# Optimization experiments

Measured on AMD Instinct MI355X. Metric: run time of the kernel, lower is better.

The kernel has to match this reference:

```python
import jax, jax.numpy as jnp
import numpy as np

N_NODES = 50000
N_EDGES = 1600000
IN_CH = 512
OUT_CH = 64
ITERATIONS = 3


def _spmm(adj_index, adj_values, x):
    # sparse @ dense: out[r] = sum_{e: row[e]==r} vals[e] * x[col[e]]
    row, col = adj_index[0], adj_index[1]
    gathered = adj_values[:, None] * x[col]  # [E, F]
    return jax.ops.segment_sum(gathered, row, num_segments=x.shape[0])


def setup_inputs() -> dict:
    key = jax.random.key(0)
    k1, k2, k3, k4, k5 = jax.random.split(key, 5)
    adj_index = jax.random.randint(k1, (2, N_EDGES), 0, N_NODES, dtype=jnp.int64)
    # positive normalized-like edge weights ~ 1/avg_degree
    adj_values = jax.random.uniform(k2, (N_EDGES,), dtype=jnp.float32) / 32.0
    features = jax.random.normal(k3, (N_NODES, IN_CH), dtype=jnp.float32)
    xavier_w = float(np.sqrt(6.0 / (IN_CH + OUT_CH)))
    weight_matrix = jax.random.uniform(k4, (IN_CH, OUT_CH), dtype=jnp.float32, minval=-xavier_w, maxval=xavier_w)
    xavier_b = float(np.sqrt(6.0 / (1 + OUT_CH)))
    bias = jax.random.uniform(k5, (1, OUT_CH), dtype=jnp.float32, minval=-xavier_b, maxval=xavier_b)
    return {"adj_index": adj_index, "adj_values": adj_values, "features": features,
            "weight_matrix": weight_matrix, "bias": bias}


def reference(adj_index, adj_values, features, weight_matrix, bias):
    # dense projection (dropout_rate=0.0 / eval mode -> identity dropout)
    base = features @ weight_matrix  # [N, OUT_CH]
    # repeated sparse-dense propagation: A^(iterations-1) @ (X W)
    for _ in range(ITERATIONS - 1):
        base = _spmm(adj_index, adj_values, base)
    return base + bias
```

## Files before the change

kernel.cpp:

```cpp
#include <hip/hip_runtime.h>
#include <hip/hip_bf16.h>

typedef __attribute__((ext_vector_type(8))) __bf16 bf16x8;
typedef __attribute__((ext_vector_type(4))) float f32x4;

#define IN_CH 512
#define OUT_CH 64
#define BS 98
#define NB 512
#define CHUNK 8192
#define CAP 4096

__device__ inline unsigned short f2bf(float f) {
    __hip_bfloat16 h = __float2bfloat16(f);
    return __builtin_bit_cast(unsigned short, h);
}

__global__ __launch_bounds__(512) void prep_kernel(
    const float* __restrict__ W, __hip_bfloat16* __restrict__ Wf,
    int* __restrict__ bcur)
{
    const int t = blockIdx.x * 512 + threadIdx.x;
    if (t < NB) bcur[t] = t * CAP;
    const int ct = t >> 10;
    const int rem = t & 1023;
    const int ks = rem >> 6;
    const int l = rem & 63;
    const int col = ct * 16 + (l & 15);
    const int kb = ks * 32 + (l >> 4) * 8;
    __hip_bfloat16* dst = Wf + (size_t)t * 8;
    #pragma unroll
    for (int j = 0; j < 8; ++j)
        dst[j] = (__hip_bfloat16)W[(size_t)(kb + j) * OUT_CH + col];
}

__global__ __launch_bounds__(128) void gemm_kernel(
    const float* __restrict__ A, const bf16x8* __restrict__ wf,
    __hip_bfloat16* __restrict__ outb, int N)
{
    __shared__ __align__(16) char Abf[32 * 1024];

    const int tid = threadIdx.x;
    const int row0 = blockIdx.x * 32;

    #pragma unroll 1
    for (int ob = 0; ob < 4; ++ob) {
        float4 v[8];
        #pragma unroll
        for (int j = 0; j < 8; ++j) {
            int f = (ob * 8 + j) * 128 + tid;
            int row = f >> 7, c4 = f & 127;
            int rg = row0 + row; rg = rg < N ? rg : N - 1;
            v[j] = *(const float4*)(A + (size_t)rg * IN_CH + c4 * 4);
        }
        #pragma unroll
        for (int j = 0; j < 8; ++j) {
            int f = (ob * 8 + j) * 128 + tid;
            int row = f >> 7, c4 = f & 127;
            int blk = c4 >> 1, half = c4 & 1;
            ushort4 h;
            h.x = f2bf(v[j].x); h.y = f2bf(v[j].y);
            h.z = f2bf(v[j].z); h.w = f2bf(v[j].w);
            *(ushort4*)(Abf + row * 1024 + ((blk ^ (row & 7)) << 4) + (half << 3)) = h;
        }
    }
    __syncthreads();

    const int lane = tid & 63;
    const int wave = tid >> 6;
    const int arow = wave * 16 + (lane & 15);
    const int kgb = lane >> 4;

    bf16x8 a[16];
    #pragma unroll
    for (int ks = 0; ks < 16; ++ks)
        a[ks] = *(const bf16x8*)(Abf + arow * 1024 +
                                 (((ks * 4 + kgb) ^ (arow & 7)) << 4));

    const int colb = lane & 15;
    const int rr = row0 + wave * 16 + (lane >> 4) * 4;
    #pragma unroll 1
    for (int ct = 0; ct < 4; ++ct) {
        bf16x8 w[16];
        #pragma unroll
        for (int ks = 0; ks < 16; ++ks) w[ks] = wf[(ct * 16 + ks) * 64 + lane];
        f32x4 acc = {0.f, 0.f, 0.f, 0.f};
        #pragma unroll
        for (int ks = 0; ks < 16; ++ks)
            acc = __builtin_amdgcn_mfma_f32_16x16x32_bf16(a[ks], w[ks], acc, 0, 0, 0);
        int col = ct * 16 + colb;
        #pragma unroll
        for (int i = 0; i < 4; ++i) {
            int r = rr + i;
            if (r < N)
                outb[(size_t)r * OUT_CH + col] = __float2bfloat16(acc[i]);
        }
    }
}

__global__ __launch_bounds__(512) void bucket_scatter_kernel(
    const int* __restrict__ rows, const int* __restrict__ cols,
    const float* __restrict__ vals, int* __restrict__ bcur,
    int2* __restrict__ seg, int E)
{
    __shared__ int hist[NB];
    __shared__ int posBase[NB];
    const int tid = threadIdx.x;
    const int base = blockIdx.x * CHUNK + tid * 16;

    hist[tid] = 0;
    __syncthreads();

    int myb[16], mypack[16]; float myval[16];
    if (base + 16 <= E) {
        int4 r4[4], c4[4]; float4 v4[4];
        #pragma unroll
        for (int q = 0; q < 4; ++q) {
            r4[q] = *(const int4*)(rows + base + q * 4);
            c4[q] = *(const int4*)(cols + base + q * 4);
            v4[q] = *(const float4*)(vals + base + q * 4);
        }
        #pragma unroll
        for (int q = 0; q < 4; ++q) {
            int rr[4] = {r4[q].x, r4[q].y, r4[q].z, r4[q].w};
            int cc[4] = {c4[q].x, c4[q].y, c4[q].z, c4[q].w};
            float vv[4] = {v4[q].x, v4[q].y, v4[q].z, v4[q].w};
            #pragma unroll
            for (int u = 0; u < 4; ++u) {
                int j = q * 4 + u;
                int r = rr[u];
                int b = r / BS;
                myb[j] = b;
                mypack[j] = (cc[u] << 8) | (r - b * BS);
                myval[j] = vv[u];
                atomicAdd(&hist[b], 1);
            }
        }
    } else {
        #pragma unroll
        for (int j = 0; j < 16; ++j) {
            int e = base + j;
            myb[j] = -1;
            if (e < E) {
                int r = rows[e];
                int b = r / BS;
                myb[j] = b;
                mypack[j] = (cols[e] << 8) | (r - b * BS);
                myval[j] = vals[e];
                atomicAdd(&hist[b], 1);
            }
        }
    }
    __syncthreads();

    int h = hist[tid];
    if (h) posBase[tid] = atomicAdd(&bcur[tid], h);
    hist[tid] = 0;
    __syncthreads();

    #pragma unroll
    for (int j = 0; j < 16; ++j) {
        if (myb[j] >= 0) {
            int p = posBase[myb[j]] + atomicAdd(&hist[myb[j]], 1);
            int2 cv; cv.x = mypack[j]; cv.y = __float_as_int(myval[j]);
            seg[p] = cv;
        }
    }
}

__global__ __launch_bounds__(512) void sort_kernel(
    const int* __restrict__ bcur, const int2* __restrict__ seg,
    unsigned* __restrict__ segc,
    int* __restrict__ offs, int* __restrict__ rend)
{
    __shared__ unsigned sorted4[CAP];
    __shared__ int hist[BS + 1];
    __shared__ int cursor[BS];

    const int b = blockIdx.x;
    const int t = threadIdx.x;
    const int s = b * CAP;
    const int cnt = bcur[b] - s;

    if (t < BS + 1) hist[t] = 0;
    __syncthreads();

    int2 ed[8];
    #pragma unroll
    for (int j = 0; j < 8; ++j) {
        int idx = t + j * 512;
        if (idx < cnt) {
            ed[j] = seg[s + idx];
            atomicAdd(&hist[ed[j].x & 255], 1);
        }
    }
    __syncthreads();

    if (t == 0) {
        int run = 0;
        for (int i = 0; i < BS; ++i) { int c = hist[i]; hist[i] = run; run += c; }
        hist[BS] = run;
    }
    __syncthreads();

    if (t < BS) {
        cursor[t] = hist[t];
        offs[b * BS + t] = s + hist[t];
        rend[b * BS + t] = s + hist[t + 1];
    }
    __syncthreads();

    #pragma unroll
    for (int j = 0; j < 8; ++j) {
        int idx = t + j * 512;
        if (idx < cnt) {
            int pos = atomicAdd(&cursor[ed[j].x & 255], 1);
            unsigned col = ((unsigned)ed[j].x) >> 8;
            sorted4[pos] = (col << 16) | f2bf(__int_as_float(ed[j].y));
        }
    }
    __syncthreads();

    #pragma unroll
    for (int j = 0; j < 8; ++j) {
        int idx = t + j * 512;
        if (idx < cnt) segc[s + idx] = sorted4[idx];
    }
}

__global__ __launch_bounds__(256) void spmm_row_kernel(
    const int* __restrict__ offs, const int* __restrict__ rend,
    const unsigned* __restrict__ segc,
    const __hip_bfloat16* __restrict__ x,
    __hip_bfloat16* __restrict__ yb,
    float* __restrict__ yf,
    const float* __restrict__ bias, int N)
{
    const int lane = threadIdx.x & 63;
    int r = blockIdx.x * 4 + (threadIdx.x >> 6);
    if (r >= N) return;
    r = __builtin_amdgcn_readfirstlane(r);

    const int s = offs[r];
    const int e = rend[r];
    const __hip_bfloat16* xl = x + lane;

    float acc = 0.f;
    int i0 = s;
    for (; i0 + 16 <= e; i0 += 16) {
        unsigned p[16];
        #pragma unroll
        for (int j = 0; j < 16; ++j) p[j] = segc[i0 + j];
        float xv[16];
        #pragma unroll
        for (int j = 0; j < 16; ++j)
            xv[j] = __bfloat162float(xl[(size_t)(p[j] >> 16) * OUT_CH]);
        #pragma unroll
        for (int j = 0; j < 16; ++j)
            acc = fmaf(__int_as_float(p[j] << 16), xv[j], acc);
    }
    if (i0 < e) {
        #pragma unroll
        for (int j = 0; j < 16; ++j) {
            int ij = i0 + j < e ? i0 + j : e - 1;
            unsigned p = segc[ij];
            float w = (i0 + j < e) ? __int_as_float(p << 16) : 0.f;
            float xv = __bfloat162float(xl[(size_t)(p >> 16) * OUT_CH]);
            acc = fmaf(w, xv, acc);
        }
    }
    if (yf) yf[(size_t)r * OUT_CH + lane] = acc + bias[lane];
    else    yb[(size_t)r * OUT_CH + lane] = __float2bfloat16(acc);
}

static inline size_t align_up(size_t v) { return (v + 255) & ~(size_t)255; }

extern "C" void kernel_launch(void* const* d_in, const int* in_sizes, int n_in,
                              void* d_out, int out_size, void* d_ws, size_t ws_size,
                              hipStream_t stream)
{
    const int*   adj  = (const int*)d_in[0];
    const float* vals = (const float*)d_in[1];
    const float* feat = (const float*)d_in[2];
    const float* Wm   = (const float*)d_in[3];
    const float* bias = (const float*)d_in[4];

    const int E = in_sizes[1];
    const int N = in_sizes[2] / IN_CH;
    const int* rows  = adj;
    const int* colsI = adj + E;

    char* w = (char*)d_ws;
    size_t o = 0;
    __hip_bfloat16* B0b = (__hip_bfloat16*)(w + o); o += align_up((size_t)N * OUT_CH * 2);
    __hip_bfloat16* Y1b = (__hip_bfloat16*)(w + o); o += align_up((size_t)N * OUT_CH * 2);
    __hip_bfloat16* Wf  = (__hip_bfloat16*)(w + o); o += align_up((size_t)IN_CH * OUT_CH * 2);
    int*      bcur = (int*)     (w + o); o += align_up(NB * sizeof(int));
    int*      offs = (int*)     (w + o); o += align_up((size_t)NB * BS * sizeof(int));
    int*      rend = (int*)     (w + o); o += align_up((size_t)NB * BS * sizeof(int));
    int2*     seg  = (int2*)    (w + o); o += align_up((size_t)NB * CAP * sizeof(int2));
    unsigned* segc = (unsigned*)(w + o); o += align_up((size_t)NB * CAP * sizeof(unsigned));
    (void)ws_size; (void)n_in; (void)out_size;

    prep_kernel<<<8, 512, 0, stream>>>(Wm, Wf, bcur);

    gemm_kernel<<<(N + 31) / 32, 128, 0, stream>>>(
        feat, (const bf16x8*)Wf, B0b, N);

    bucket_scatter_kernel<<<(E + CHUNK - 1) / CHUNK, 512, 0, stream>>>(
        rows, colsI, vals, bcur, seg, E);
    sort_kernel<<<NB, 512, 0, stream>>>(bcur, seg, segc, offs, rend);

    spmm_row_kernel<<<(N + 3) / 4, 256, 0, stream>>>(
        offs, rend, segc, B0b, Y1b, nullptr, nullptr, N);
    spmm_row_kernel<<<(N + 3) / 4, 256, 0, stream>>>(
        offs, rend, segc, Y1b, nullptr, (float*)d_out, bias, N);
}
```

Before: 125.1 us.

## Process four rows per wave with 16 lanes each using vectorized bf16 gathers

```diff
diff --git a/kernel.cpp b/kernel.cpp
--- a/kernel.cpp
+++ b/kernel.cpp
@@ -14,6 +14,9 @@
 __device__ inline unsigned short f2bf(float f) {
     __hip_bfloat16 h = __float2bfloat16(f);
     return __builtin_bit_cast(unsigned short, h);
+}
+__device__ inline float bf2f(unsigned short u) {
+    return __uint_as_float(((unsigned)u) << 16);
 }
 
 __global__ __launch_bounds__(512) void prep_kernel(
@@ -236,41 +239,63 @@
     float* __restrict__ yf,
     const float* __restrict__ bias, int N)
 {
-    const int lane = threadIdx.x & 63;
-    int r = blockIdx.x * 4 + (threadIdx.x >> 6);
-    if (r >= N) return;
-    r = __builtin_amdgcn_readfirstlane(r);
-
-    const int s = offs[r];
-    const int e = rend[r];
-    const __hip_bfloat16* xl = x + lane;
-
-    float acc = 0.f;
-    int i0 = s;
-    for (; i0 + 16 <= e; i0 += 16) {
+    const int tid = threadIdx.x;
+    const int lane = tid & 63;
+    const int wave = tid >> 6;
+    const int grp = lane >> 4;
+    const int l16 = lane & 15;
+
+    int r = (blockIdx.x * 4 + wave) * 4 + grp;
+    const bool rv = r < N;
+    const int rc = rv ? r : N - 1;
+    const int s = offs[rc];
+    const int e = rv ? rend[rc] : s;
+
+    int m = e - s;
+    m = max(m, __shfl_xor(m, 16));
+    m = max(m, __shfl_xor(m, 32));
+    const int iters = (m + 15) >> 4;
+
+    const ushort* xp = (const ushort*)x + l16 * 4;
+
+    float4 acc = {0.f, 0.f, 0.f, 0.f};
+    for (int it = 0; it < iters; ++it) {
+        const int base = s + it * 16;
         unsigned p[16];
         #pragma unroll
-        for (int j = 0; j < 16; ++j) p[j] = segc[i0 + j];
-        float xv[16];
+        for (int j = 0; j < 16; ++j) {
+            int idx = base + j;
+            p[j] = segc[idx < e ? idx : s];
+        }
+        ushort4 xv[16];
         #pragma unroll
         for (int j = 0; j < 16; ++j)
-            xv[j] = __bfloat162float(xl[(size_t)(p[j] >> 16) * OUT_CH]);
-        #pragma unroll
-        for (int j = 0; j < 16; ++j)
-            acc = fmaf(__int_as_float(p[j] << 16), xv[j], acc);
-    }
-    if (i0 < e) {
+            xv[j] = *(const ushort4*)(xp + (size_t)(p[j] >> 16) * OUT_CH);
         #pragma unroll
         for (int j = 0; j < 16; ++j) {
-            int ij = i0 + j < e ? i0 + j : e - 1;
-            unsigned p = segc[ij];
-            float w = (i0 + j < e) ? __int_as_float(p << 16) : 0.f;
-            float xv = __bfloat162float(xl[(size_t)(p >> 16) * OUT_CH]);
-            acc = fmaf(w, xv, acc);
-        }
-    }
-    if (yf) yf[(size_t)r * OUT_CH + lane] = acc + bias[lane];
-    else    yb[(size_t)r * OUT_CH + lane] = __float2bfloat16(acc);
+            int idx = base + j;
+            float wv = (idx < e) ? __uint_as_float(p[j] << 16) : 0.f;
+            acc.x = fmaf(wv, bf2f(xv[j].x), acc.x);
+            acc.y = fmaf(wv, bf2f(xv[j].y), acc.y);
+            acc.z = fmaf(wv, bf2f(xv[j].z), acc.z);
+            acc.w = fmaf(wv, bf2f(xv[j].w), acc.w);
+        }
+    }
+
+    if (rv) {
+        if (yf) {
+            float4 bv = *(const float4*)(bias + l16 * 4);
+            float4 o;
+            o.x = acc.x + bv.x; o.y = acc.y + bv.y;
+            o.z = acc.z + bv.z; o.w = acc.w + bv.w;
+            *(float4*)(yf + (size_t)r * OUT_CH + l16 * 4) = o;
+        } else {
+            ushort4 h;
+            h.x = f2bf(acc.x); h.y = f2bf(acc.y);
+            h.z = f2bf(acc.z); h.w = f2bf(acc.w);
+            *(ushort4*)((ushort*)yb + (size_t)r * OUT_CH + l16 * 4) = h;
+        }
+    }
 }
 
 static inline size_t align_up(size_t v) { return (v + 255) & ~(size_t)255; }
@@ -311,8 +336,9 @@
         rows, colsI, vals, bcur, seg, E);
     sort_kernel<<<NB, 512, 0, stream>>>(bcur, seg, segc, offs, rend);
 
-    spmm_row_kernel<<<(N + 3) / 4, 256, 0, stream>>>(
+    const int rows_per_block = 16;
+    spmm_row_kernel<<<(N + rows_per_block - 1) / rows_per_block, 256, 0, stream>>>(
         offs, rend, segc, B0b, Y1b, nullptr, nullptr, N);
-    spmm_row_kernel<<<(N + 3) / 4, 256, 0, stream>>>(
+    spmm_row_kernel<<<(N + rows_per_block - 1) / rows_per_block, 256, 0, stream>>>(
         offs, rend, segc, Y1b, nullptr, (float*)d_out, bias, N);
 }
```

Result: faster. 117.8 us (-5.8%).
